# Optimization experiments

Hardware: AMD Instinct MI355X
Metric: run time of the kernel (lower is better)

## Reference

```python
import jax, jax.numpy as jnp
import numpy as np

GRID_RES_SAMPLE = 0.08  # config.grid_resolution_sample
VOXEL_SIZE = 0.04       # scene voxel size encoded in transforms


def setup_inputs() -> dict:
    key = jax.random.key(0)
    ks = jax.random.split(key, 4)
    B, X = 4, 96
    G = 192            # == ceil(X * GRID_RES_SAMPLE / VOXEL_SIZE), matches dynamic size_voxel_grid
    N = 500_000        # sparse occupied voxels per scene
    NUM_ADD = 5000     # static stand-in for occ_grids.sum()+100 mask augmentations
    # scene voxel-grid transform: scale VOXEL_SIZE, translate -5m (same structure per scene)
    T = np.eye(4, dtype=np.float32)
    T[0, 0] = T[1, 1] = T[2, 2] = VOXEL_SIZE
    T[:3, 3] = -5.0
    transforms = np.tile(T, (B, 1, 1)).astype(np.float32)
    transforms_inv = np.stack([np.linalg.inv(t) for t in transforms]).astype(np.float32)
    # per-batch regular coordinate grids with random world offsets in [0,1)m
    offs = np.asarray(jax.random.uniform(ks[0], (B, 3), dtype=jnp.float32))
    ax = np.arange(X, dtype=np.float32) * GRID_RES_SAMPLE
    gx, gy, gz = np.meshgrid(ax, ax, ax, indexing='ij')
    base = np.stack([gx, gy, gz], axis=0)  # [3,X,X,X]
    coords = (base[None] + offs[:, :, None, None, None]).astype(np.float32)
    sparse = jax.random.randint(ks[1], (B, N, 3), 0, 400, dtype=jnp.int32)
    rand_idx = jax.random.randint(ks[2], (3, NUM_ADD), 0, X, dtype=jnp.int32)
    conv_w = jnp.ones((1, 1, 5, 5, 5), jnp.float32)  # Conv3d(1,1,5) all-ones, no bias
    return {
        'coordinate_grids': jnp.asarray(coords),
        'transforms': jnp.asarray(transforms),
        'transforms_inv': jnp.asarray(transforms_inv),
        'sparse_encoding': sparse,
        'conv_w': conv_w,
        'rand_idx': rand_idx,
        'grid_size': G,
    }


def reference(coordinate_grids, transforms, transforms_inv, sparse_encoding, conv_w, rand_idx, grid_size):
    B, C, X, Y, Z = coordinate_grids.shape
    flat = coordinate_grids.reshape(B, 3, -1)
    min_loc = flat.min(-1)   # [B,3]
    max_loc = flat.max(-1)   # [B,3]
    max_size_grid = (max_loc + GRID_RES_SAMPLE - min_loc).max(0)  # [3]
    min_homo = jnp.concatenate([min_loc, jnp.ones((B, 1), flat.dtype)], axis=1)
    min_voxel_idx = jnp.floor(jnp.einsum('bij,bj->bi', transforms_inv, min_homo)[:, :3])
    min_voxel_idx = jnp.maximum(min_voxel_idx, 0.0)  # [B,3]
    size_vox = jnp.ceil(jnp.einsum('bij,j->bi', transforms_inv[:, :3, :3], max_size_grid).max(0))  # [3], == grid_size
    # shift sparse indices into the local window and filter out-of-range ones
    se = sparse_encoding.astype(jnp.float32) - min_voxel_idx[:, None, :]   # [B,N,3]
    valid = ((se >= 0) & (se < size_vox)).all(-1)                          # [B,N]
    sei = jnp.clip(se.astype(jnp.int32), 0, grid_size - 1)
    occ = jnp.zeros((B, grid_size, grid_size, grid_size), jnp.float32)
    b_idx = jnp.broadcast_to(jnp.arange(B)[:, None], valid.shape)
    occ = occ.at[b_idx, sei[..., 0], sei[..., 1], sei[..., 2]].max(valid.astype(jnp.float32))
    # world position of voxel (0,0,0) of the local window and window extent
    min_homo_idx = jnp.concatenate([min_voxel_idx, jnp.ones((B, 1), flat.dtype)], axis=1)
    pos_base = jnp.einsum('bij,bj->bi', transforms, min_homo_idx)[:, :3]   # [B,3]
    extent = jnp.einsum('bij,j->bi', transforms[:, :3, :3], size_vox)      # [B,3]
    voxel_size = extent / size_vox                                          # [B,3]
    # trilinear interpolation of dense occ grid at the coordinate grid (voxel-center convention)
    p = (coordinate_grids - pos_base[:, :, None, None, None]) / voxel_size[:, :, None, None, None] - 0.5
    p0 = jnp.floor(p)
    f = p - p0                       # [B,3,X,Y,Z]
    p0 = p0.astype(jnp.int32)
    bb = jnp.arange(B)[:, None, None, None]
    out = jnp.zeros((B, X, Y, Z), jnp.float32)
    for dx in (0, 1):
        for dy in (0, 1):
            for dz in (0, 1):
                ix = jnp.clip(p0[:, 0] + dx, 0, grid_size - 1)
                iy = jnp.clip(p0[:, 1] + dy, 0, grid_size - 1)
                iz = jnp.clip(p0[:, 2] + dz, 0, grid_size - 1)
                w = ((f[:, 0] if dx else 1 - f[:, 0]) *
                     (f[:, 1] if dy else 1 - f[:, 1]) *
                     (f[:, 2] if dz else 1 - f[:, 2]))
                out = out + w * occ[bb, ix, iy, iz]
    occ_grids = out[:, None]  # [B,1,X,Y,Z]
    # 5x5x5 all-ones conv mask
    conv = jax.lax.conv_general_dilated(
        occ_grids, conv_w, window_strides=(1, 1, 1),
        padding=[(2, 2), (2, 2), (2, 2)],
        dimension_numbers=('NCDHW', 'OIDHW', 'NCDHW'))
    mask = conv > 0
    # random-index mask augmentation (num_voxels_to_add fixed statically)
    num_add = rand_idx.shape[1]
    badd = jnp.arange(num_add) % B
    mask = mask.at[badd, 0, rand_idx[0], rand_idx[1], rand_idx[2]].set(True)
    return occ_grids.astype(bool), mask
```

## Files before the change

### kernel.cpp

```cpp
#include <hip/hip_runtime.h>
#include <math.h>

#define GS   192
#define XS   96
#define XS3  (XS*XS*XS)
#define GRS  0.08f

#define PI_OFF     256
#define PF_OFF     (256 + 1152*4)
#define OCC_OFF    16384
#define OCC_WORDS  (4*GS*GS*(GS/32))
#define OUT_OFF    (OCC_OFF + OCC_WORDS*4)
#define OUTB_WORDS (4*XS*XS*(XS/32))

__device__ __forceinline__ int clampi(int v, int lo, int hi) {
    return v < lo ? lo : (v > hi ? hi : v);
}

__global__ void k_scalars(const float* __restrict__ coords,
                          const float* __restrict__ T,
                          const float* __restrict__ Tinv,
                          float* ws, int B) {
    __shared__ int imn[12], imx[12];
    __shared__ float SS[64];
    int t = threadIdx.x;
    if (t < 12) { imn[t] = 0x7F800000; imx[t] = 0; }
    __syncthreads();
    int tot = B * 3 * XS;
    for (int e = t; e < tot; e += 256) {
        int b = e / (3 * XS); int c = (e / XS) % 3; int i = e % XS;
        size_t off = (size_t)(b*3 + c) * XS3
                   + (c == 0 ? (size_t)i * XS * XS : (c == 1 ? (size_t)i * XS : (size_t)i));
        int v = __float_as_int(coords[off]);
        atomicMin(&imn[b*3 + c], v);
        atomicMax(&imx[b*3 + c], v);
    }
    __syncthreads();
    if (t == 0) {
        float mnl[12], mxl[12];
        for (int k = 0; k < 12; k++) { mnl[k] = __int_as_float(imn[k]); mxl[k] = __int_as_float(imx[k]); }
        float msg[3];
        for (int c = 0; c < 3; c++) {
            float m = -__builtin_inff();
            for (int b = 0; b < B; b++) {
                float v = __fadd_rn(mxl[b*3 + c], GRS);
                v = __fsub_rn(v, mnl[b*3 + c]);
                m = fmaxf(m, v);
            }
            msg[c] = m;
        }
        for (int b = 0; b < B; b++)
            for (int i = 0; i < 3; i++) {
                const float* R = Tinv + b*16 + i*4;
                float v = __fmul_rn(R[0], mnl[b*3 + 0]);
                v = __fadd_rn(v, __fmul_rn(R[1], mnl[b*3 + 1]));
                v = __fadd_rn(v, __fmul_rn(R[2], mnl[b*3 + 2]));
                v = __fadd_rn(v, R[3]);
                SS[24 + b*3 + i] = fmaxf(floorf(v), 0.0f);
            }
        for (int i = 0; i < 3; i++) {
            float m = -__builtin_inff();
            for (int b = 0; b < B; b++) {
                const float* R = Tinv + b*16 + i*4;
                float v = __fmul_rn(R[0], msg[0]);
                v = __fadd_rn(v, __fmul_rn(R[1], msg[1]));
                v = __fadd_rn(v, __fmul_rn(R[2], msg[2]));
                m = fmaxf(m, v);
            }
            SS[36 + i] = ceilf(m);
        }
        for (int b = 0; b < B; b++)
            for (int i = 0; i < 3; i++) {
                const float* R = T + b*16 + i*4;
                float v = __fmul_rn(R[0], SS[24 + b*3 + 0]);
                v = __fadd_rn(v, __fmul_rn(R[1], SS[24 + b*3 + 1]));
                v = __fadd_rn(v, __fmul_rn(R[2], SS[24 + b*3 + 2]));
                v = __fadd_rn(v, R[3]);
                SS[40 + b*3 + i] = v;
            }
        for (int b = 0; b < B; b++)
            for (int i = 0; i < 3; i++) {
                const float* R = T + b*16 + i*4;
                float v = __fmul_rn(R[0], SS[36 + 0]);
                v = __fadd_rn(v, __fmul_rn(R[1], SS[36 + 1]));
                v = __fadd_rn(v, __fmul_rn(R[2], SS[36 + 2]));
                SS[52 + b*3 + i] = v / SS[36 + i];
            }
        for (int k = 24; k < 64; k++) ws[k] = SS[k];
    }
    __syncthreads();
    int* PI = (int*)((char*)ws + PI_OFF);
    float* PF = (float*)((char*)ws + PF_OFF);
    for (int e = t; e < tot; e += 256) {
        int b = e / (3 * XS); int c = (e / XS) % 3; int i = e % XS;
        size_t off = (size_t)(b*3 + c) * XS3
                   + (c == 0 ? (size_t)i * XS * XS : (c == 1 ? (size_t)i * XS : (size_t)i));
        float v = coords[off];
        float p = (v - SS[40 + b*3 + c]) / SS[52 + b*3 + c] - 0.5f;
        float p0 = floorf(p);
        PI[e] = (int)p0;
        PF[e] = p - p0;
    }
}

__global__ void k_scatter(const int* __restrict__ sparse, const float* __restrict__ ws,
                          unsigned* __restrict__ occ, int N, int total) {
    int t = blockIdx.x * blockDim.x + threadIdx.x;
    if (t >= total) return;
    int b = t / N;
    const float* S = ws;
    int s0 = sparse[(size_t)t*3 + 0];
    int s1 = sparse[(size_t)t*3 + 1];
    int s2 = sparse[(size_t)t*3 + 2];
    float e0 = (float)s0 - S[24 + b*3 + 0];
    float e1 = (float)s1 - S[24 + b*3 + 1];
    float e2 = (float)s2 - S[24 + b*3 + 2];
    if (e0 >= 0.f && e0 < S[36+0] && e1 >= 0.f && e1 < S[36+1] && e2 >= 0.f && e2 < S[36+2]) {
        int x = clampi((int)e0, 0, GS-1);
        int y = clampi((int)e1, 0, GS-1);
        int z = clampi((int)e2, 0, GS-1);
        atomicOr(&occ[(((size_t)b*GS + x)*GS + y)*(GS/32) + (z >> 5)], 1u << (z & 31));
    }
}

__global__ __launch_bounds__(256) void k_interp(const float* __restrict__ ws,
                                                const unsigned* __restrict__ occ,
                                                int* __restrict__ out0,
                                                unsigned* __restrict__ outb,
                                                int total) {
    int gid = blockIdx.x * 256 + threadIdx.x;
    if (gid >= total) return;
    int z = gid % XS;
    int r1 = gid / XS;
    int y = r1 % XS;
    int r2 = r1 / XS;
    int x = r2 % XS;
    int b = r2 / XS;
    const int* PI = (const int*)((const char*)ws + PI_OFF);
    const float* PF = (const float*)((const char*)ws + PF_OFF);
    int ix = PI[(b*3 + 0)*XS + x]; float fx = PF[(b*3 + 0)*XS + x];
    int iy = PI[(b*3 + 1)*XS + y]; float fy = PF[(b*3 + 1)*XS + y];
    int iz = PI[(b*3 + 2)*XS + z]; float fz = PF[(b*3 + 2)*XS + z];
    int x0 = clampi(ix,   0, GS-1), x1 = clampi(ix+1, 0, GS-1);
    int y0 = clampi(iy,   0, GS-1), y1 = clampi(iy+1, 0, GS-1);
    int z0 = clampi(iz,   0, GS-1), z1 = clampi(iz+1, 0, GS-1);
    float wx0 = 1.f - fx, wx1 = fx, wy0 = 1.f - fy, wy1 = fy, wz0 = 1.f - fz, wz1 = fz;
    const unsigned* r00 = occ + (((size_t)b*GS + x0)*GS + y0)*(GS/32);
    const unsigned* r01 = occ + (((size_t)b*GS + x0)*GS + y1)*(GS/32);
    const unsigned* r10 = occ + (((size_t)b*GS + x1)*GS + y0)*(GS/32);
    const unsigned* r11 = occ + (((size_t)b*GS + x1)*GS + y1)*(GS/32);
    float w00 = wx0*wy0, w01 = wx0*wy1, w10 = wx1*wy0, w11 = wx1*wy1;
    float s = 0.f;
    s += w00*wz0*(float)((r00[z0>>5] >> (z0&31)) & 1u);
    s += w00*wz1*(float)((r00[z1>>5] >> (z1&31)) & 1u);
    s += w01*wz0*(float)((r01[z0>>5] >> (z0&31)) & 1u);
    s += w01*wz1*(float)((r01[z1>>5] >> (z1&31)) & 1u);
    s += w10*wz0*(float)((r10[z0>>5] >> (z0&31)) & 1u);
    s += w10*wz1*(float)((r10[z1>>5] >> (z1&31)) & 1u);
    s += w11*wz0*(float)((r11[z0>>5] >> (z0&31)) & 1u);
    s += w11*wz1*(float)((r11[z1>>5] >> (z1&31)) & 1u);
    bool nz = (s != 0.f);
    out0[gid] = nz ? 1 : 0;
    unsigned long long m = __ballot(nz);
    int lane = threadIdx.x & 63;
    if (lane == 0)  outb[gid >> 5] = (unsigned)m;
    if (lane == 32) outb[gid >> 5] = (unsigned)(m >> 32);
}

__global__ __launch_bounds__(256) void k_dilate_bits(const unsigned* __restrict__ outb,
                                                     unsigned* __restrict__ outb2,
                                                     int totalW) {
    int t = blockIdx.x * 256 + threadIdx.x;
    if (t >= totalW) return;
    int w = t % 3;
    int r1 = t / 3;
    int j = r1 % XS;
    int r2 = r1 / XS;
    int i = r2 % XS;
    int b = r2 / XS;
    unsigned accP = 0, accC = 0, accN = 0;
    for (int di = -2; di <= 2; di++) {
        int ii = i + di; if (ii < 0 || ii >= XS) continue;
        for (int dj = -2; dj <= 2; dj++) {
            int jj = j + dj; if (jj < 0 || jj >= XS) continue;
            const unsigned* row = outb + ((size_t)(b*XS + ii)*XS + jj)*3;
            accC |= row[w];
            if (w > 0) accP |= row[w-1];
            if (w < 2) accN |= row[w+1];
        }
    }
    unsigned d = accC
               | (accC << 1) | (accP >> 31)
               | (accC << 2) | (accP >> 30)
               | (accC >> 1) | (accN << 31)
               | (accC >> 2) | (accN << 30);
    outb2[t] = d;
}

__global__ __launch_bounds__(256) void k_expand(const unsigned* __restrict__ outb2,
                                                int* __restrict__ out1, int total) {
    int gid = blockIdx.x * 256 + threadIdx.x;
    if (gid >= total) return;
    out1[gid] = (int)((outb2[gid >> 5] >> (gid & 31)) & 1u);
}

__global__ void k_rand(const int* __restrict__ rand_idx, int* __restrict__ maskout,
                       int nadd, int B) {
    int i = blockIdx.x * blockDim.x + threadIdx.x;
    if (i >= nadd) return;
    int b = i % B;
    int r0 = rand_idx[i], r1 = rand_idx[nadd + i], r2 = rand_idx[2*nadd + i];
    maskout[((size_t)(b*XS + r0)*XS + r1)*XS + r2] = 1;
}

extern "C" void kernel_launch(void* const* d_in, const int* in_sizes, int n_in,
                              void* d_out, int out_size, void* d_ws, size_t ws_size,
                              hipStream_t stream) {
    const float* coords = (const float*)d_in[0];
    const float* T      = (const float*)d_in[1];
    const float* Tinv   = (const float*)d_in[2];
    const int*   sparse = (const int*)d_in[3];
    const int*   rand_i = (const int*)d_in[5];
    int* out = (int*)d_out;

    int B = in_sizes[1] / 16;
    int N = in_sizes[3] / (B * 3);
    int nadd = in_sizes[5] / 3;

    float*    ws    = (float*)d_ws;
    unsigned* occ   = (unsigned*)((char*)d_ws + OCC_OFF);
    unsigned* outb  = (unsigned*)((char*)d_ws + OUT_OFF);
    unsigned* outb2 = (unsigned*)((char*)d_ws + OCC_OFF);
    size_t half = (size_t)B * XS3;

    hipMemsetAsync((char*)d_ws + OCC_OFF, 0, (size_t)OCC_WORDS * 4, stream);

    k_scalars<<<1, 256, 0, stream>>>(coords, T, Tinv, ws, B);
    int totalPts = B * N;
    k_scatter<<<(totalPts + 255) / 256, 256, 0, stream>>>(sparse, ws, occ, N, totalPts);
    int total = B * XS3;
    k_interp<<<(total + 255) / 256, 256, 0, stream>>>(ws, occ, out, outb, total);
    int totalW = B * XS * XS * 3;
    k_dilate_bits<<<(totalW + 255) / 256, 256, 0, stream>>>(outb, outb2, totalW);
    k_expand<<<(total + 255) / 256, 256, 0, stream>>>(outb2, out + half, total);
    k_rand<<<(nadd + 255) / 256, 256, 0, stream>>>(rand_i, out + half, nadd, B);
}
```

Measured before the change: 153.9 us.

## Fuse zeroing, random-mask scatter, and dilate+expand to cut kernel launches

Replaces the memset with zeroing inside the init kernel. The random-index mask is folded into a bitmask built during the scatter kernel. The dilate and expand kernels are merged so each block dilates 256 words into shared memory and writes the expanded int mask, ORing in the random bits. This removes three launches and the intermediate dilated-bit round trip through global memory. In exchange, one init block now also carries the serial scalar work alongside the zeroing blocks.

```diff
diff --git a/kernel.cpp b/kernel.cpp
--- a/kernel.cpp
+++ b/kernel.cpp
@@ -5,6 +5,7 @@
 #define XS   96
 #define XS3  (XS*XS*XS)
 #define GRS  0.08f
+#define NTHR 256
 
 #define PI_OFF     256
 #define PF_OFF     (256 + 1152*4)
@@ -12,22 +13,30 @@
 #define OCC_WORDS  (4*GS*GS*(GS/32))
 #define OUT_OFF    (OCC_OFF + OCC_WORDS*4)
 #define OUTB_WORDS (4*XS*XS*(XS/32))
+#define RM_OFF     (OUT_OFF + OUTB_WORDS*4)
+#define ZERO_UINT4 ((OCC_WORDS + 2*OUTB_WORDS) / 4)
 
 __device__ __forceinline__ int clampi(int v, int lo, int hi) {
     return v < lo ? lo : (v > hi ? hi : v);
 }
 
-__global__ void k_scalars(const float* __restrict__ coords,
-                          const float* __restrict__ T,
-                          const float* __restrict__ Tinv,
-                          float* ws, int B) {
-    __shared__ int imn[12], imx[12];
+__global__ __launch_bounds__(256) void k_init(const float* __restrict__ coords,
+                                              const float* __restrict__ T,
+                                              const float* __restrict__ Tinv,
+                                              float* ws, int B) {
+    int gtid = blockIdx.x * NTHR + threadIdx.x;
+    uint4* zp = (uint4*)((char*)ws + OCC_OFF);
+    if (gtid < ZERO_UINT4) zp[gtid] = make_uint4(0u, 0u, 0u, 0u);
+
+    if (blockIdx.x != 0) return;
+
+    __shared__ int   imn[12], imx[12];
     __shared__ float SS[64];
     int t = threadIdx.x;
     if (t < 12) { imn[t] = 0x7F800000; imx[t] = 0; }
     __syncthreads();
     int tot = B * 3 * XS;
-    for (int e = t; e < tot; e += 256) {
+    for (int e = t; e < tot; e += NTHR) {
         int b = e / (3 * XS); int c = (e / XS) % 3; int i = e % XS;
         size_t off = (size_t)(b*3 + c) * XS3
                    + (c == 0 ? (size_t)i * XS * XS : (c == 1 ? (size_t)i * XS : (size_t)i));
@@ -91,7 +100,7 @@
     __syncthreads();
     int* PI = (int*)((char*)ws + PI_OFF);
     float* PF = (float*)((char*)ws + PF_OFF);
-    for (int e = t; e < tot; e += 256) {
+    for (int e = t; e < tot; e += NTHR) {
         int b = e / (3 * XS); int c = (e / XS) % 3; int i = e % XS;
         size_t off = (size_t)(b*3 + c) * XS3
                    + (c == 0 ? (size_t)i * XS * XS : (c == 1 ? (size_t)i * XS : (size_t)i));
@@ -103,9 +112,19 @@
     }
 }
 
-__global__ void k_scatter(const int* __restrict__ sparse, const float* __restrict__ ws,
-                          unsigned* __restrict__ occ, int N, int total) {
-    int t = blockIdx.x * blockDim.x + threadIdx.x;
+__global__ __launch_bounds__(256) void k_scatter(const int* __restrict__ sparse,
+                                                 const int* __restrict__ rand_idx,
+                                                 float* ws, int N, int total,
+                                                 int nadd, int B) {
+    int t = blockIdx.x * NTHR + threadIdx.x;
+    unsigned* occ   = (unsigned*)((char*)ws + OCC_OFF);
+    unsigned* rmask = (unsigned*)((char*)ws + RM_OFF);
+    if (t < nadd) {
+        int b = t % B;
+        int r0 = rand_idx[t], r1 = rand_idx[nadd + t], r2 = rand_idx[2*nadd + t];
+        int g = ((b*XS + r0)*XS + r1)*XS + r2;
+        atomicOr(&rmask[g >> 5], 1u << (g & 31));
+    }
     if (t >= total) return;
     int b = t / N;
     const float* S = ws;
@@ -124,12 +143,12 @@
 }
 
 __global__ __launch_bounds__(256) void k_interp(const float* __restrict__ ws,
-                                                const unsigned* __restrict__ occ,
                                                 int* __restrict__ out0,
                                                 unsigned* __restrict__ outb,
                                                 int total) {
-    int gid = blockIdx.x * 256 + threadIdx.x;
+    int gid = blockIdx.x * NTHR + threadIdx.x;
     if (gid >= total) return;
+    const unsigned* occ = (const unsigned*)((const char*)ws + OCC_OFF);
     int z = gid % XS;
     int r1 = gid / XS;
     int y = r1 % XS;
@@ -167,17 +186,20 @@
     if (lane == 32) outb[gid >> 5] = (unsigned)(m >> 32);
 }
 
-__global__ __launch_bounds__(256) void k_dilate_bits(const unsigned* __restrict__ outb,
-                                                     unsigned* __restrict__ outb2,
-                                                     int totalW) {
-    int t = blockIdx.x * 256 + threadIdx.x;
-    if (t >= totalW) return;
+__global__ __launch_bounds__(256) void k_dilate_expand(const float* __restrict__ ws,
+                                                       int* __restrict__ out1) {
+    __shared__ unsigned dsm[NTHR];
+    const unsigned* outb  = (const unsigned*)((const char*)ws + OUT_OFF);
+    const unsigned* rmask = (const unsigned*)((const char*)ws + RM_OFF);
+    int chunk = blockIdx.x;
+    int tid = threadIdx.x;
+    int t = chunk * NTHR + tid;
     int w = t % 3;
-    int r1 = t / 3;
-    int j = r1 % XS;
-    int r2 = r1 / XS;
-    int i = r2 % XS;
-    int b = r2 / XS;
+    int rr1 = t / 3;
+    int j = rr1 % XS;
+    int rr2 = rr1 / XS;
+    int i = rr2 % XS;
+    int b = rr2 / XS;
     unsigned accP = 0, accC = 0, accN = 0;
     for (int di = -2; di <= 2; di++) {
         int ii = i + di; if (ii < 0 || ii >= XS) continue;
@@ -194,23 +216,12 @@
                | (accC << 2) | (accP >> 30)
                | (accC >> 1) | (accN << 31)
                | (accC >> 2) | (accN << 30);
-    outb2[t] = d;
-}
-
-__global__ __launch_bounds__(256) void k_expand(const unsigned* __restrict__ outb2,
-                                                int* __restrict__ out1, int total) {
-    int gid = blockIdx.x * 256 + threadIdx.x;
-    if (gid >= total) return;
-    out1[gid] = (int)((outb2[gid >> 5] >> (gid & 31)) & 1u);
-}
-
-__global__ void k_rand(const int* __restrict__ rand_idx, int* __restrict__ maskout,
-                       int nadd, int B) {
-    int i = blockIdx.x * blockDim.x + threadIdx.x;
-    if (i >= nadd) return;
-    int b = i % B;
-    int r0 = rand_idx[i], r1 = rand_idx[nadd + i], r2 = rand_idx[2*nadd + i];
-    maskout[((size_t)(b*XS + r0)*XS + r1)*XS + r2] = 1;
+    d |= rmask[t];
+    dsm[tid] = d;
+    __syncthreads();
+    int base = chunk * (NTHR * 32);
+    for (int k = 0; k < 32; k++)
+        out1[base + k*NTHR + tid] = (int)((dsm[k*8 + (tid >> 5)] >> (tid & 31)) & 1u);
 }
 
 extern "C" void kernel_launch(void* const* d_in, const int* in_sizes, int n_in,
@@ -227,21 +238,15 @@
     int N = in_sizes[3] / (B * 3);
     int nadd = in_sizes[5] / 3;
 
-    float*    ws    = (float*)d_ws;
-    unsigned* occ   = (unsigned*)((char*)d_ws + OCC_OFF);
-    unsigned* outb  = (unsigned*)((char*)d_ws + OUT_OFF);
-    unsigned* outb2 = (unsigned*)((char*)d_ws + OCC_OFF);
+    float*    ws   = (float*)d_ws;
+    unsigned* outb = (unsigned*)((char*)d_ws + OUT_OFF);
     size_t half = (size_t)B * XS3;
 
-    hipMemsetAsync((char*)d_ws + OCC_OFF, 0, (size_t)OCC_WORDS * 4, stream);
-
-    k_scalars<<<1, 256, 0, stream>>>(coords, T, Tinv, ws, B);
+    k_init<<<ZERO_UINT4 / NTHR, NTHR, 0, stream>>>(coords, T, Tinv, ws, B);
     int totalPts = B * N;
-    k_scatter<<<(totalPts + 255) / 256, 256, 0, stream>>>(sparse, ws, occ, N, totalPts);
+    k_scatter<<<(totalPts + NTHR - 1) / NTHR, NTHR, 0, stream>>>(sparse, rand_i, ws,
+                                                                 N, totalPts, nadd, B);
     int total = B * XS3;
-    k_interp<<<(total + 255) / 256, 256, 0, stream>>>(ws, occ, out, outb, total);
-    int totalW = B * XS * XS * 3;
-    k_dilate_bits<<<(totalW + 255) / 256, 256, 0, stream>>>(outb, outb2, totalW);
-    k_expand<<<(total + 255) / 256, 256, 0, stream>>>(outb2, out + half, total);
-    k_rand<<<(nadd + 255) / 256, 256, 0, stream>>>(rand_i, out + half, nadd, B);
-}
+    k_interp<<<total / NTHR, NTHR, 0, stream>>>(ws, out, outb, total);
+    k_dilate_expand<<<(B * XS * XS * 3) / NTHR, NTHR, 0, stream>>>(ws, out + half);
+}
```

New measurement: 146.8 us. 1.05x faster.
